# Kernel tuning notes

Measured on AMD Instinct MI355X. Metric: run time of the kernel, lower is better.

Reference implementation:

```python
import jax, jax.numpy as jnp
import numpy as np

IN_DIM = 128
HIDDEN = 128


def setup_inputs() -> dict:
    key = jax.random.key(0)
    k1, k2, k3, k4, k5 = jax.random.split(key, 5)
    bound_ih = 1.0 / np.sqrt(IN_DIM)
    bound_hh = 1.0 / np.sqrt(HIDDEN)
    return {
        "x": jax.random.normal(k1, (256, 2048, IN_DIM), dtype=jnp.float32),
        "W_ih": jax.random.uniform(k2, (HIDDEN, IN_DIM), minval=-bound_ih, maxval=bound_ih, dtype=jnp.float32),
        "b_ih": jax.random.uniform(k3, (HIDDEN,), minval=-bound_ih, maxval=bound_ih, dtype=jnp.float32),
        "W_hh": jax.random.uniform(k4, (HIDDEN, HIDDEN), minval=-bound_hh, maxval=bound_hh, dtype=jnp.float32),
        "b_hh": jax.random.uniform(k5, (HIDDEN,), minval=-bound_hh, maxval=bound_hh, dtype=jnp.float32),
    }


def reference(x, W_ih, b_ih, W_hh, b_hh):
    B, S, _ = x.shape
    # Precompute input projection for all timesteps in one big GEMM: [B,S,H]
    xw = jnp.einsum("bsi,hi->bsh", x, W_ih) + b_ih
    h0 = jnp.zeros((B, W_hh.shape[0]), dtype=x.dtype)

    def step(h, xw_t):
        h_new = jnp.tanh(xw_t + h @ W_hh.T + b_hh)
        return h_new, None

    # scan over time axis: move S to leading dim
    h_final, _ = jax.lax.scan(step, h0, jnp.swapaxes(xw, 0, 1))
    return h_final
```

## Files before the change

### kernel.cpp

```cpp
#include <hip/hip_runtime.h>


#define BATCH 256
#define SEQ   2048
#define HID   128
#define CH    16
#define NCHUNK (SEQ / CH)

template <int CTRL>
__device__ __forceinline__ float dpp_movf(float x) {
    return __int_as_float(__builtin_amdgcn_mov_dpp(__float_as_int(x), CTRL, 0xF, 0xF, true));
}

__device__ __forceinline__ float tanh_fast(float x) {
    x = fminf(fmaxf(x, -12.0f), 12.0f);
    float e = __expf(2.0f * x);
    return 1.0f - __fdividef(2.0f, e + 1.0f);
}

__global__ __launch_bounds__(256, 1) void rnn_scan_kernel(
    const float* __restrict__ x,
    const float* __restrict__ Wih,
    const float* __restrict__ bih,
    const float* __restrict__ Whh,
    const float* __restrict__ bhh,
    float* __restrict__ out)
{
    const int b = blockIdx.x;
    const int t = threadIdx.x;
    const int g = t >> 4;
    const int c = t & 15;
    const int colbase = c << 3;
    const int rowbase = g << 3;

    __shared__ __align__(16) float xbuf[2][CH * HID];
    __shared__ __align__(16) float hbuf[2][192];

    float4 wi[8][2], wh[8][2];
#pragma unroll
    for (int r = 0; r < 8; ++r) {
        const float* pi = Wih + (rowbase + r) * HID + colbase;
        const float* ph = Whh + (rowbase + r) * HID + colbase;
        wi[r][0] = *(const float4*)(pi);
        wi[r][1] = *(const float4*)(pi + 4);
        wh[r][0] = *(const float4*)(ph);
        wh[r][1] = *(const float4*)(ph + 4);
    }

    const int m = c & 3;
    const int o = ((m & 1) << 2) | (m & 2);
    const int row0 = rowbase + o;
    const float bias0 = bih[row0] + bhh[row0];
    const float bias1 = bih[row0 + 1] + bhh[row0 + 1];
    const int hw = row0 + (g << 2);

    const float* xsrc = x + (size_t)b * (SEQ * HID);

    {
        const float4* gp = (const float4*)xsrc;
        float4 p0 = gp[t];
        float4 p1 = gp[256 + t];
        float4* lb = (float4*)&xbuf[0][0];
        lb[t] = p0;
        lb[256 + t] = p1;
    }
    if (t < 192) hbuf[0][t] = 0.0f;
    __syncthreads();

    int cur = 0;
    for (int chn = 0; chn < NCHUNK; ++chn) {
        float4 q0, q1;
        const bool pf = (chn + 1 < NCHUNK);
        if (pf) {
            const float4* gp = (const float4*)(xsrc + (size_t)(chn + 1) * (CH * HID));
            q0 = gp[t];
            q1 = gp[256 + t];
        }
        const float* xb = &xbuf[chn & 1][0];
#pragma unroll 1
        for (int s = 0; s < CH; ++s) {
            const float* xr = xb + s * HID + colbase;
            const float* hr = &hbuf[cur][12 * c];
            float4 xv0 = *(const float4*)(xr);
            float4 xv1 = *(const float4*)(xr + 4);
            float4 hv0 = *(const float4*)(hr);
            float4 hv1 = *(const float4*)(hr + 4);

            float a[8];
#pragma unroll
            for (int r = 0; r < 8; ++r) {
                float acc;
                acc = wi[r][0].x * xv0.x;
                acc = fmaf(wi[r][0].y, xv0.y, acc);
                acc = fmaf(wi[r][0].z, xv0.z, acc);
                acc = fmaf(wi[r][0].w, xv0.w, acc);
                acc = fmaf(wi[r][1].x, xv1.x, acc);
                acc = fmaf(wi[r][1].y, xv1.y, acc);
                acc = fmaf(wi[r][1].z, xv1.z, acc);
                acc = fmaf(wi[r][1].w, xv1.w, acc);
                acc = fmaf(wh[r][0].x, hv0.x, acc);
                acc = fmaf(wh[r][0].y, hv0.y, acc);
                acc = fmaf(wh[r][0].z, hv0.z, acc);
                acc = fmaf(wh[r][0].w, hv0.w, acc);
                acc = fmaf(wh[r][1].x, hv1.x, acc);
                acc = fmaf(wh[r][1].y, hv1.y, acc);
                acc = fmaf(wh[r][1].z, hv1.z, acc);
                acc = fmaf(wh[r][1].w, hv1.w, acc);
                a[r] = acc;
            }

            const bool b0 = (c & 1) != 0;
            const bool b1 = (c & 2) != 0;
            float k0 = b0 ? a[4] : a[0], g0 = b0 ? a[0] : a[4];
            float k1 = b0 ? a[5] : a[1], g1 = b0 ? a[1] : a[5];
            float k2 = b0 ? a[6] : a[2], g2 = b0 ? a[2] : a[6];
            float k3 = b0 ? a[7] : a[3], g3 = b0 ? a[3] : a[7];
            float t0 = k0 + dpp_movf<0xB1>(g0);
            float t1 = k1 + dpp_movf<0xB1>(g1);
            float t2 = k2 + dpp_movf<0xB1>(g2);
            float t3 = k3 + dpp_movf<0xB1>(g3);
            float k4 = b1 ? t2 : t0, g4 = b1 ? t0 : t2;
            float k5 = b1 ? t3 : t1, g5 = b1 ? t1 : t3;
            float u0 = k4 + dpp_movf<0x4E>(g4);
            float u1 = k5 + dpp_movf<0x4E>(g5);
            u0 += dpp_movf<0x124>(u0);
            u1 += dpp_movf<0x124>(u1);
            u0 += dpp_movf<0x128>(u0);
            u1 += dpp_movf<0x128>(u1);

            float h0 = tanh_fast(u0 + bias0);
            float h1 = tanh_fast(u1 + bias1);
            if (c < 4) {
                *(float2*)&hbuf[cur ^ 1][hw] = make_float2(h0, h1);
            }

            if (s == CH - 1 && pf) {
                float4* lb = (float4*)&xbuf[(chn + 1) & 1][0];
                lb[t] = q0;
                lb[256 + t] = q1;
            }
            __syncthreads();
            cur ^= 1;
        }
    }
    if (t < HID) out[(size_t)b * HID + t] = hbuf[cur][t + ((t >> 3) << 2)];
}

extern "C" void kernel_launch(void* const* d_in, const int* in_sizes, int n_in,
                              void* d_out, int out_size, void* d_ws, size_t ws_size,
                              hipStream_t stream) {
    const float* x   = (const float*)d_in[0];
    const float* Wih = (const float*)d_in[1];
    const float* bih = (const float*)d_in[2];
    const float* Whh = (const float*)d_in[3];
    const float* bhh = (const float*)d_in[4];
    float* out = (float*)d_out;

    rnn_scan_kernel<<<BATCH, 256, 0, stream>>>(x, Wih, bih, Whh, bhh, out);
}
```

Before: 1.302 ms.

## Double threads per block to 512, halving rows per thread in RNN scan

Each block now uses 512 threads, and each thread handles 4 hidden rows instead of 8, which halves the serial FMA chain and register use per thread. The DPP reduction tree shrinks by one level. The x-chunk staging is swizzled in LDS to avoid bank conflicts on the new access pattern. The intent is to shorten the per-timestep latency of the sequential recurrence, at the cost of more waves contending for each per-step __syncthreads barrier.

```diff
diff --git a/kernel.cpp b/kernel.cpp
--- a/kernel.cpp
+++ b/kernel.cpp
@@ -18,7 +18,7 @@
     return 1.0f - __fdividef(2.0f, e + 1.0f);
 }
 
-__global__ __launch_bounds__(256, 1) void rnn_scan_kernel(
+__global__ __launch_bounds__(512, 2) void rnn_scan_kernel(
     const float* __restrict__ x,
     const float* __restrict__ Wih,
     const float* __restrict__ bih,
@@ -31,14 +31,14 @@
     const int g = t >> 4;
     const int c = t & 15;
     const int colbase = c << 3;
-    const int rowbase = g << 3;
+    const int rowbase = g << 2;
 
     __shared__ __align__(16) float xbuf[2][CH * HID];
     __shared__ __align__(16) float hbuf[2][192];
 
-    float4 wi[8][2], wh[8][2];
+    float4 wi[4][2], wh[4][2];
 #pragma unroll
-    for (int r = 0; r < 8; ++r) {
+    for (int r = 0; r < 4; ++r) {
         const float* pi = Wih + (rowbase + r) * HID + colbase;
         const float* ph = Whh + (rowbase + r) * HID + colbase;
         wi[r][0] = *(const float4*)(pi);
@@ -48,47 +48,46 @@
     }
 
     const int m = c & 3;
-    const int o = ((m & 1) << 2) | (m & 2);
+    const int o = ((m & 1) << 1) | ((m >> 1) & 1);
     const int row0 = rowbase + o;
-    const float bias0 = bih[row0] + bhh[row0];
-    const float bias1 = bih[row0 + 1] + bhh[row0 + 1];
-    const int hw = row0 + (g << 2);
+    const float bias = bih[row0] + bhh[row0];
+    const int hw = row0 + ((row0 >> 3) << 2);
+
+    const int bx = (c >> 2) & 1;
+    const int xoff0 = (((c << 1) ^ bx) << 2);
+    const int xoff1 = ((((c << 1) | 1) ^ bx) << 2);
+    const int sidx = t ^ ((t >> 3) & 1);
 
     const float* xsrc = x + (size_t)b * (SEQ * HID);
 
     {
         const float4* gp = (const float4*)xsrc;
-        float4 p0 = gp[t];
-        float4 p1 = gp[256 + t];
-        float4* lb = (float4*)&xbuf[0][0];
-        lb[t] = p0;
-        lb[256 + t] = p1;
+        ((float4*)&xbuf[0][0])[sidx] = gp[t];
     }
     if (t < 192) hbuf[0][t] = 0.0f;
     __syncthreads();
 
     int cur = 0;
     for (int chn = 0; chn < NCHUNK; ++chn) {
-        float4 q0, q1;
+        float4 q0;
         const bool pf = (chn + 1 < NCHUNK);
         if (pf) {
             const float4* gp = (const float4*)(xsrc + (size_t)(chn + 1) * (CH * HID));
             q0 = gp[t];
-            q1 = gp[256 + t];
         }
         const float* xb = &xbuf[chn & 1][0];
 #pragma unroll 1
         for (int s = 0; s < CH; ++s) {
-            const float* xr = xb + s * HID + colbase;
+            const float* xr = xb + s * HID;
             const float* hr = &hbuf[cur][12 * c];
-            float4 xv0 = *(const float4*)(xr);
-            float4 xv1 = *(const float4*)(xr + 4);
             float4 hv0 = *(const float4*)(hr);
             float4 hv1 = *(const float4*)(hr + 4);
+            float4 xv0 = *(const float4*)(xr + xoff0);
+            float4 xv1 = *(const float4*)(xr + xoff1);
 
-            float a[8];
+            float a[4];
 #pragma unroll
-            for (int r = 0; r < 8; ++r) {
+            for (int r = 0; r < 4; ++r) {
                 float acc;
                 acc = wi[r][0].x * xv0.x;
                 acc = fmaf(wi[r][0].y, xv0.y, acc);
@@ -111,33 +110,22 @@
 
             const bool b0 = (c & 1) != 0;
             const bool b1 = (c & 2) != 0;
-            float k0 = b0 ? a[4] : a[0], g0 = b0 ? a[0] : a[4];
-            float k1 = b0 ? a[5] : a[1], g1 = b0 ? a[1] : a[5];
-            float k2 = b0 ? a[6] : a[2], g2 = b0 ? a[2] : a[6];
-            float k3 = b0 ? a[7] : a[3], g3 = b0 ? a[3] : a[7];
-            float t0 = k0 + dpp_movf<0xB1>(g0);
-            float t1 = k1 + dpp_movf<0xB1>(g1);
-            float t2 = k2 + dpp_movf<0xB1>(g2);
-            float t3 = k3 + dpp_movf<0xB1>(g3);
-            float k4 = b1 ? t2 : t0, g4 = b1 ? t0 : t2;
-            float k5 = b1 ? t3 : t1, g5 = b1 ? t1 : t3;
-            float u0 = k4 + dpp_movf<0x4E>(g4);
-            float u1 = k5 + dpp_movf<0x4E>(g5);
-            u0 += dpp_movf<0x124>(u0);
-            u1 += dpp_movf<0x124>(u1);
-            u0 += dpp_movf<0x128>(u0);
-            u1 += dpp_movf<0x128>(u1);
+            float k0 = b0 ? a[2] : a[0], s0 = b0 ? a[0] : a[2];
+            float k1 = b0 ? a[3] : a[1], s1 = b0 ? a[1] : a[3];
+            float t0 = k0 + dpp_movf<0xB1>(s0);
+            float t1 = k1 + dpp_movf<0xB1>(s1);
+            float k2 = b1 ? t1 : t0, s2 = b1 ? t0 : t1;
+            float u = k2 + dpp_movf<0x4E>(s2);
+            u += dpp_movf<0x124>(u);
+            u += dpp_movf<0x128>(u);
 
-            float h0 = tanh_fast(u0 + bias0);
-            float h1 = tanh_fast(u1 + bias1);
+            float h = tanh_fast(u + bias);
             if (c < 4) {
-                *(float2*)&hbuf[cur ^ 1][hw] = make_float2(h0, h1);
+                hbuf[cur ^ 1][hw] = h;
             }
 
             if (s == CH - 1 && pf) {
-                float4* lb = (float4*)&xbuf[(chn + 1) & 1][0];
-                lb[t] = q0;
-                lb[256 + t] = q1;
+                ((float4*)&xbuf[(chn + 1) & 1][0])[sidx] = q0;
             }
             __syncthreads();
             cur ^= 1;
@@ -156,5 +144,5 @@
     const float* bhh = (const float*)d_in[4];
     float* out = (float*)d_out;
 
-    rnn_scan_kernel<<<BATCH, 256, 0, stream>>>(x, Wih, bih, Whh, bhh, out);
+    rnn_scan_kernel<<<BATCH, 512, 0, stream>>>(x, Wih, bih, Whh, bhh, out);
 }
```

Result: faster. 1.106 ms (-15.0%).
